# Performance work log

Measured on AMD Instinct MI355X. Metric: run time of the kernel, lower is better.

Reference implementation:

```python
import jax, jax.numpy as jnp
import numpy as np

# Fixed varlen layout: 2 sequences of length 2048 packed into N=4096 tokens
B, S, H, HK, D = 2, 2048, 32, 8, 128
G = H // HK  # GQA group size
SCALE = 1.0 / float(np.sqrt(D))


def setup_inputs() -> dict:
    key = jax.random.key(0)
    k0, k1, k2 = jax.random.split(key, 3)
    N = B * S
    return {
        "q": jax.random.normal(k0, (N, H, D), jnp.float32),
        "k": jax.random.normal(k1, (N, HK, D), jnp.float32),
        "v": jax.random.normal(k2, (N, HK, D), jnp.float32),
        "k_cache": jnp.zeros((N, HK * D), jnp.float32),
        "v_cache": jnp.zeros((N, HK * D), jnp.float32),
        "slot_mapping": jnp.arange(N, dtype=jnp.int32),
    }


def reference(q, k, v, k_cache, v_cache, slot_mapping):
    N = q.shape[0]
    num_slots = k_cache.shape[0]
    # --- store_kvcache: scatter flattened K/V rows into paged slots; slot==-1 skipped ---
    safe = jnp.where(slot_mapping >= 0, slot_mapping, num_slots)  # out-of-range -> dropped
    k_cache_new = k_cache.at[safe].set(k.reshape(N, HK * D), mode="drop")
    v_cache_new = v_cache.at[safe].set(v.reshape(N, HK * D), mode="drop")
    # --- prefill path (block_tables=None): causal varlen attention on fresh k,v ---
    qb = q.reshape(B, S, HK, G, D)
    kb = k.reshape(B, S, HK, D)
    vb = v.reshape(B, S, HK, D)
    scores = jnp.einsum("bqhgd,bkhd->bhgqk", qb, kb) * SCALE  # [B,HK,G,S,S]
    causal = jnp.tril(jnp.ones((S, S), dtype=bool))
    scores = jnp.where(causal, scores, jnp.finfo(scores.dtype).min)
    p = jax.nn.softmax(scores, axis=-1)
    o = jnp.einsum("bhgqk,bkhd->bqhgd", p, vb).reshape(N, H, D)
    return o, k_cache_new, v_cache_new
```

## Files before the change

### kernel.cpp

```cpp
#include <hip/hip_runtime.h>
#include <stdint.h>
#include <math.h>

constexpr int B = 2, S = 2048, H = 32, HK = 8, D = 128;
constexpr int N = B * S;
constexpr int KVD = HK * D;
constexpr float SCALE = 0.08838834764831845f;
constexpr float LOG2E = 1.4426950408889634f;
constexpr float QSCALE = SCALE * LOG2E;
constexpr float CSHIFT = 8.0f;

typedef __attribute__((ext_vector_type(8))) short short8;
typedef __attribute__((ext_vector_type(4))) float floatx4;

static __device__ __forceinline__ uint32_t f2bf1(float f) {
    union { float f; uint32_t u; } c; c.f = f;
    return (c.u + 0x7FFFu + ((c.u >> 16) & 1u)) >> 16;
}
static __device__ __forceinline__ uint32_t packbf(float a, float b) {
    return f2bf1(a) | (f2bf1(b) << 16);
}
static __device__ __forceinline__ uint32_t fbits(float f) {
    union { float f; uint32_t u; } c; c.f = f; return c.u;
}
static __device__ __forceinline__ uint32_t packtrunc(float lo, float hi) {
    return __builtin_amdgcn_perm(fbits(hi), fbits(lo), 0x07060302u);
}
static __device__ __forceinline__ void load_lds16(const void* g, void* l) {
    __builtin_amdgcn_global_load_lds((const __attribute__((address_space(1))) uint32_t*)g,
                                     (__attribute__((address_space(3))) uint32_t*)l,
                                     16, 0, 0);
}

__global__ __launch_bounds__(256) void k_prep(const float* __restrict__ k,
                                              const int* __restrict__ slot_mapping,
                                              float* __restrict__ kc_out,
                                              uint16_t* __restrict__ Kb) {
    int tid = blockIdx.x * 256 + threadIdx.x;
    int idx = tid * 4;
    int token = idx >> 10;
    int rem = idx & 1023;
    float4 val = *(const float4*)(k + idx);
    int s = slot_mapping[token];
    if (s >= 0 && s < N) {
        *(float4*)(kc_out + (size_t)s * KVD + rem) = val;
    }
    int b  = token >> 11;
    int ss = token & 2047;
    int hk = rem >> 7;
    int d  = rem & 127;
    uint2 pk;
    pk.x = packbf(val.x, val.y);
    pk.y = packbf(val.z, val.w);
    *(uint2*)(Kb + (((size_t)(b * HK + hk) * S + ss) * D + d)) = pk;
}

__global__ __launch_bounds__(256) void v_prep(const float* __restrict__ v,
                                              const int* __restrict__ slot_mapping,
                                              float* __restrict__ vc_out,
                                              uint16_t* __restrict__ Vt) {
    __shared__ float tile[64][129];
    int t = threadIdx.x;
    int kv0 = blockIdx.x * 64;
    int bhk = blockIdx.y;
    int b = bhk >> 3, hk = bhk & 7;

#pragma unroll
    for (int i = 0; i < 8; ++i) {
        int r = i * 8 + (t >> 5);
        int c = (t & 31) * 4;
        int token = b * S + kv0 + r;
        float4 val = *(const float4*)(v + (size_t)token * KVD + hk * D + c);
        int s = slot_mapping[token];
        if (s >= 0 && s < N) {
            *(float4*)(vc_out + (size_t)s * KVD + hk * D + c) = val;
        }
        tile[r][c + 0] = val.x; tile[r][c + 1] = val.y;
        tile[r][c + 2] = val.z; tile[r][c + 3] = val.w;
    }
    __syncthreads();
#pragma unroll
    for (int i = 0; i < 8; ++i) {
        int d = i * 16 + (t >> 4);
        int c = (t & 15) * 4;
        uint2 pk;
        pk.x = packbf(tile[c + 0][d], tile[c + 1][d]);
        pk.y = packbf(tile[c + 2][d], tile[c + 3][d]);
        *(uint2*)(Vt + ((size_t)(bhk * D + d)) * S + kv0 + c) = pk;
    }
}

__global__ __launch_bounds__(512, 2) void attn(const float* __restrict__ q,
                                               const uint16_t* __restrict__ Kb,
                                               const uint16_t* __restrict__ Vt,
                                               float* __restrict__ out) {
    __shared__ uint16_t sK[2][64 * 128];
    __shared__ uint16_t sV[2][128 * 64];

    int id = blockIdx.x;
    int hk = id & 7;
    int s0 = id >> 3;
    int x  = s0 & 7;
    int g2 = (s0 >> 3) & 1;
    int b  = s0 >> 4;
    int h0 = hk * 4 + g2 * 2;

    int t = threadIdx.x;
    int lane = t & 63, wave = t >> 6;
    int quad = lane >> 4, n = lane & 15, xr = n & 7;

    const uint16_t* Kbh = Kb + (size_t)(b * HK + hk) * S * D;
    const uint16_t* Vbh = Vt + (size_t)(b * HK + hk) * D * S;

    const uint16_t* gK[2]; const uint16_t* gV[2];
    int oK[2], oV[2];
#pragma unroll
    for (int j = 0; j < 2; ++j) {
        int i = wave * 2 + j;
        int rK = i * 4 + (lane >> 4);
        int cK = ((lane & 15) ^ (rK & 7)) * 8;
        gK[j] = Kbh + (size_t)rK * D + cK;
        oK[j] = i * 512;
        int rV = i * 8 + (lane >> 3);
        int cV = ((lane & 7) ^ (rV & 7)) * 8;
        gV[j] = Vbh + (size_t)rV * S + cV;
        oV[j] = i * 512;
    }

    for (int pass = 0; pass < 2; ++pass) {
        int qt = pass ? x : 15 - x;
        int q0 = qt * 128;
        int qwave = q0 + wave * 16;

        short8 bq[2][4];
#pragma unroll
        for (int g = 0; g < 2; ++g) {
            const float* qrow = q + (size_t)(b * S + qwave + n) * (H * D) + (h0 + g) * D + quad * 8;
#pragma unroll
            for (int kc = 0; kc < 4; ++kc) {
                float4 v0 = *(const float4*)(qrow + kc * 32);
                float4 v1 = *(const float4*)(qrow + kc * 32 + 4);
                uint4 pk;
                pk.x = packtrunc(v0.x * QSCALE, v0.y * QSCALE);
                pk.y = packtrunc(v0.z * QSCALE, v0.w * QSCALE);
                pk.z = packtrunc(v1.x * QSCALE, v1.y * QSCALE);
                pk.w = packtrunc(v1.z * QSCALE, v1.w * QSCALE);
                bq[g][kc] = *(short8*)&pk;
            }
        }

        floatx4 o_acc[2][8];
#pragma unroll
        for (int g = 0; g < 2; ++g)
#pragma unroll
            for (int i = 0; i < 8; ++i) o_acc[g][i] = (floatx4){0.f, 0.f, 0.f, 0.f};
        float lsum[2] = {0.f, 0.f};

        int nt = 2 * qt + 2;
        __syncthreads();
#pragma unroll
        for (int j = 0; j < 2; ++j) load_lds16(gK[j], &sK[0][0] + oK[j]);
#pragma unroll
        for (int j = 0; j < 2; ++j) load_lds16(gV[j], &sV[0][0] + oV[j]);

        for (int tile = 0; tile < nt; ++tile) {
            int cur = tile & 1;
            __syncthreads();
            if (tile + 1 < nt) {
                int kvn = (tile + 1) * 64;
#pragma unroll
                for (int j = 0; j < 2; ++j) load_lds16(gK[j] + (size_t)kvn * D, &sK[cur ^ 1][0] + oK[j]);
#pragma unroll
                for (int j = 0; j < 2; ++j) load_lds16(gV[j] + kvn, &sV[cur ^ 1][0] + oV[j]);
            }
            int kv0 = tile * 64;
            if (kv0 > qwave + 15) continue;

            const uint16_t* K_ = &sK[cur][0];
            const uint16_t* V_ = &sV[cur][0];

            floatx4 acc[2][4];
#pragma unroll
            for (int g = 0; g < 2; ++g)
#pragma unroll
                for (int sub = 0; sub < 4; ++sub) acc[g][sub] = (floatx4){0.f, 0.f, 0.f, 0.f};
#pragma unroll
            for (int sub = 0; sub < 4; ++sub) {
#pragma unroll
                for (int kc = 0; kc < 4; ++kc) {
                    short8 ak = *(const short8*)(K_ + (sub * 16 + n) * 128 + (((kc * 4 + quad) ^ xr) * 8));
                    acc[0][sub] = __builtin_amdgcn_mfma_f32_16x16x32_bf16(ak, bq[0][kc], acc[0][sub], 0, 0, 0);
                    acc[1][sub] = __builtin_amdgcn_mfma_f32_16x16x32_bf16(ak, bq[1][kc], acc[1][sub], 0, 0, 0);
                }
            }

            short8 ap[2][2];
            int qg = qwave + n;
            if (kv0 + 63 > qwave) {
#pragma unroll
                for (int sub = 0; sub < 4; ++sub)
#pragma unroll
                    for (int reg = 0; reg < 4; ++reg)
                        if (kv0 + sub * 16 + quad * 4 + reg > qg) {
                            acc[0][sub][reg] = -1e9f;
                            acc[1][sub][reg] = -1e9f;
                        }
            }
#pragma unroll
            for (int g = 0; g < 2; ++g) {
                float rs = 0.f;
                uint32_t pw[4][2];
#pragma unroll
                for (int sub = 0; sub < 4; ++sub) {
                    float p0 = exp2f(acc[g][sub][0] - CSHIFT);
                    float p1 = exp2f(acc[g][sub][1] - CSHIFT);
                    float p2 = exp2f(acc[g][sub][2] - CSHIFT);
                    float p3 = exp2f(acc[g][sub][3] - CSHIFT);
                    rs += (p0 + p1) + (p2 + p3);
                    pw[sub][0] = packtrunc(p0, p1);
                    pw[sub][1] = packtrunc(p2, p3);
                }
                lsum[g] += rs;

#pragma unroll
                for (int ks = 0; ks < 2; ++ks) {
                    uint32_t x0 = pw[2 * ks][0],     x1 = pw[2 * ks][1];
                    uint32_t y0 = pw[2 * ks + 1][0], y1 = pw[2 * ks + 1][1];
                    asm("v_permlane32_swap_b32 %0, %1" : "+v"(x0), "+v"(y0));
                    asm("v_permlane32_swap_b32 %0, %1" : "+v"(x1), "+v"(y1));
                    asm("v_permlane16_swap_b32 %0, %1" : "+v"(x0), "+v"(y0));
                    asm("v_permlane16_swap_b32 %0, %1" : "+v"(x1), "+v"(y1));
                    uint4 w; w.x = x0; w.y = x1; w.z = y0; w.w = y1;
                    ap[g][ks] = *(short8*)&w;
                }
            }

#pragma unroll
            for (int d8 = 0; d8 < 8; ++d8) {
#pragma unroll
                for (int ks = 0; ks < 2; ++ks) {
                    short8 bv = *(const short8*)(V_ + (d8 * 16 + n) * 64 + (((ks * 4 + quad) ^ xr) * 8));
                    o_acc[0][d8] = __builtin_amdgcn_mfma_f32_16x16x32_bf16(ap[0][ks], bv, o_acc[0][d8], 0, 0, 0);
                    o_acc[1][d8] = __builtin_amdgcn_mfma_f32_16x16x32_bf16(ap[1][ks], bv, o_acc[1][d8], 0, 0, 0);
                }
            }
        }

#pragma unroll
        for (int g = 0; g < 2; ++g) {
            float s = lsum[g];
            s += __shfl_xor(s, 16);
            s += __shfl_xor(s, 32);
            float linv = 1.0f / s;
            float lr[4];
#pragma unroll
            for (int reg = 0; reg < 4; ++reg) lr[reg] = __shfl(linv, quad * 4 + reg);
#pragma unroll
            for (int d8 = 0; d8 < 8; ++d8) {
#pragma unroll
                for (int reg = 0; reg < 4; ++reg) {
                    size_t row = (size_t)(b * S + qwave + quad * 4 + reg);
                    out[row * (H * D) + (h0 + g) * D + d8 * 16 + n] = o_acc[g][d8][reg] * lr[reg];
                }
            }
        }
    }
}

extern "C" void kernel_launch(void* const* d_in, const int* in_sizes, int n_in,
                              void* d_out, int out_size, void* d_ws, size_t ws_size,
                              hipStream_t stream) {
    const float* q = (const float*)d_in[0];
    const float* k = (const float*)d_in[1];
    const float* v = (const float*)d_in[2];
    const int* slot_mapping = (const int*)d_in[5];

    float* o_out  = (float*)d_out;
    float* kc_out = o_out + (size_t)N * H * D;
    float* vc_out = kc_out + (size_t)N * KVD;

    uint16_t* Kb = (uint16_t*)d_ws;
    uint16_t* Vt = Kb + (size_t)B * HK * S * D;

    k_prep<<<(N * KVD / 4) / 256, 256, 0, stream>>>(k, slot_mapping, kc_out, Kb);
    v_prep<<<dim3(S / 64, B * HK), 256, 0, stream>>>(v, slot_mapping, vc_out, Vt);
    attn<<<dim3(256), 512, 0, stream>>>(q, Kb, Vt, o_out);
}
```

Before: 282.3 us.

## Software-pipeline QK and softmax-PV across 32-wide KV tiles with 4-buffer LDS

Shrinks KV tiles from 64 to 32 rows, keeps four LDS buffers, and interleaves the QK^T MFMA of one tile with the softmax and PV of the previous tile, so exp and VALU work can overlap matrix-core work. The V tile layout and swizzle are changed to fit the narrower tile, and each wave now issues a single global-to-LDS load per tile. This adds twice as many barriers per KV row and more register pressure from the two live score accumulators, which could hurt occupancy at 2 blocks of 512 threads.

```diff
diff --git a/kernel.cpp b/kernel.cpp
--- a/kernel.cpp
+++ b/kernel.cpp
@@ -94,8 +94,8 @@
                                                const uint16_t* __restrict__ Kb,
                                                const uint16_t* __restrict__ Vt,
                                                float* __restrict__ out) {
-    __shared__ uint16_t sK[2][64 * 128];
-    __shared__ uint16_t sV[2][128 * 64];
+    __shared__ uint16_t sK[4][32 * 128];
+    __shared__ uint16_t sV[4][128 * 32];
 
     int id = blockIdx.x;
     int hk = id & 7;
@@ -112,20 +112,14 @@
     const uint16_t* Kbh = Kb + (size_t)(b * HK + hk) * S * D;
     const uint16_t* Vbh = Vt + (size_t)(b * HK + hk) * D * S;
 
-    const uint16_t* gK[2]; const uint16_t* gV[2];
-    int oK[2], oV[2];
-#pragma unroll
-    for (int j = 0; j < 2; ++j) {
-        int i = wave * 2 + j;
-        int rK = i * 4 + (lane >> 4);
-        int cK = ((lane & 15) ^ (rK & 7)) * 8;
-        gK[j] = Kbh + (size_t)rK * D + cK;
-        oK[j] = i * 512;
-        int rV = i * 8 + (lane >> 3);
-        int cV = ((lane & 7) ^ (rV & 7)) * 8;
-        gV[j] = Vbh + (size_t)rV * S + cV;
-        oV[j] = i * 512;
-    }
+    int rK = wave * 4 + (lane >> 4);
+    int cK = ((lane & 15) ^ (rK & 7)) * 8;
+    const uint16_t* gK = Kbh + (size_t)rK * D + cK;
+    int oK = wave * 512;
+    int rV = wave * 16 + (lane >> 2);
+    int cV = ((lane & 3) ^ ((lane >> 3) & 3)) * 8;
+    const uint16_t* gV = Vbh + (size_t)rV * S + cV;
+    int oV = wave * 512;
 
     for (int pass = 0; pass < 2; ++pass) {
         int qt = pass ? x : 15 - x;
@@ -156,36 +150,22 @@
             for (int i = 0; i < 8; ++i) o_acc[g][i] = (floatx4){0.f, 0.f, 0.f, 0.f};
         float lsum[2] = {0.f, 0.f};
 
-        int nt = 2 * qt + 2;
-        __syncthreads();
-#pragma unroll
-        for (int j = 0; j < 2; ++j) load_lds16(gK[j], &sK[0][0] + oK[j]);
-#pragma unroll
-        for (int j = 0; j < 2; ++j) load_lds16(gV[j], &sV[0][0] + oV[j]);
-
-        for (int tile = 0; tile < nt; ++tile) {
-            int cur = tile & 1;
-            __syncthreads();
-            if (tile + 1 < nt) {
-                int kvn = (tile + 1) * 64;
-#pragma unroll
-                for (int j = 0; j < 2; ++j) load_lds16(gK[j] + (size_t)kvn * D, &sK[cur ^ 1][0] + oK[j]);
-#pragma unroll
-                for (int j = 0; j < 2; ++j) load_lds16(gV[j] + kvn, &sV[cur ^ 1][0] + oV[j]);
-            }
-            int kv0 = tile * 64;
-            if (kv0 > qwave + 15) continue;
-
-            const uint16_t* K_ = &sK[cur][0];
-            const uint16_t* V_ = &sV[cur][0];
-
-            floatx4 acc[2][4];
+        auto STAGE = [&](int tile) {
+            int buf = tile & 3;
+            size_t kvn = (size_t)tile * 32;
+            load_lds16(gK + kvn * D, &sK[buf][0] + oK);
+            load_lds16(gV + kvn, &sV[buf][0] + oV);
+        };
+        auto QK = [&](int tile, floatx4 (&acc)[2][2]) {
+            int kv0 = tile * 32;
 #pragma unroll
             for (int g = 0; g < 2; ++g)
 #pragma unroll
-                for (int sub = 0; sub < 4; ++sub) acc[g][sub] = (floatx4){0.f, 0.f, 0.f, 0.f};
-#pragma unroll
-            for (int sub = 0; sub < 4; ++sub) {
+                for (int sub = 0; sub < 2; ++sub) acc[g][sub] = (floatx4){0.f, 0.f, 0.f, 0.f};
+            if (kv0 > qwave + 15) return;
+            const uint16_t* K_ = &sK[tile & 3][0];
+#pragma unroll
+            for (int sub = 0; sub < 2; ++sub) {
 #pragma unroll
                 for (int kc = 0; kc < 4; ++kc) {
                     short8 ak = *(const short8*)(K_ + (sub * 16 + n) * 128 + (((kc * 4 + quad) ^ xr) * 8));
@@ -193,12 +173,15 @@
                     acc[1][sub] = __builtin_amdgcn_mfma_f32_16x16x32_bf16(ak, bq[1][kc], acc[1][sub], 0, 0, 0);
                 }
             }
-
-            short8 ap[2][2];
+        };
+        auto SMPV = [&](int tile, floatx4 (&acc)[2][2]) {
+            int kv0 = tile * 32;
+            if (kv0 > qwave + 15) return;
+            const uint16_t* V_ = &sV[tile & 3][0];
             int qg = qwave + n;
-            if (kv0 + 63 > qwave) {
-#pragma unroll
-                for (int sub = 0; sub < 4; ++sub)
+            if (kv0 + 31 > qwave) {
+#pragma unroll
+                for (int sub = 0; sub < 2; ++sub)
 #pragma unroll
                     for (int reg = 0; reg < 4; ++reg)
                         if (kv0 + sub * 16 + quad * 4 + reg > qg) {
@@ -206,12 +189,13 @@
                             acc[1][sub][reg] = -1e9f;
                         }
             }
+            short8 ap[2];
 #pragma unroll
             for (int g = 0; g < 2; ++g) {
                 float rs = 0.f;
-                uint32_t pw[4][2];
-#pragma unroll
-                for (int sub = 0; sub < 4; ++sub) {
+                uint32_t pw[2][2];
+#pragma unroll
+                for (int sub = 0; sub < 2; ++sub) {
                     float p0 = exp2f(acc[g][sub][0] - CSHIFT);
                     float p1 = exp2f(acc[g][sub][1] - CSHIFT);
                     float p2 = exp2f(acc[g][sub][2] - CSHIFT);
@@ -221,30 +205,41 @@
                     pw[sub][1] = packtrunc(p2, p3);
                 }
                 lsum[g] += rs;
-
-#pragma unroll
-                for (int ks = 0; ks < 2; ++ks) {
-                    uint32_t x0 = pw[2 * ks][0],     x1 = pw[2 * ks][1];
-                    uint32_t y0 = pw[2 * ks + 1][0], y1 = pw[2 * ks + 1][1];
-                    asm("v_permlane32_swap_b32 %0, %1" : "+v"(x0), "+v"(y0));
-                    asm("v_permlane32_swap_b32 %0, %1" : "+v"(x1), "+v"(y1));
-                    asm("v_permlane16_swap_b32 %0, %1" : "+v"(x0), "+v"(y0));
-                    asm("v_permlane16_swap_b32 %0, %1" : "+v"(x1), "+v"(y1));
-                    uint4 w; w.x = x0; w.y = x1; w.z = y0; w.w = y1;
-                    ap[g][ks] = *(short8*)&w;
-                }
-            }
-
+                uint32_t x0 = pw[0][0], x1 = pw[0][1];
+                uint32_t y0 = pw[1][0], y1 = pw[1][1];
+                asm("v_permlane32_swap_b32 %0, %1" : "+v"(x0), "+v"(y0));
+                asm("v_permlane32_swap_b32 %0, %1" : "+v"(x1), "+v"(y1));
+                asm("v_permlane16_swap_b32 %0, %1" : "+v"(x0), "+v"(y0));
+                asm("v_permlane16_swap_b32 %0, %1" : "+v"(x1), "+v"(y1));
+                uint4 w; w.x = x0; w.y = x1; w.z = y0; w.w = y1;
+                ap[g] = *(short8*)&w;
+            }
 #pragma unroll
             for (int d8 = 0; d8 < 8; ++d8) {
-#pragma unroll
-                for (int ks = 0; ks < 2; ++ks) {
-                    short8 bv = *(const short8*)(V_ + (d8 * 16 + n) * 64 + (((ks * 4 + quad) ^ xr) * 8));
-                    o_acc[0][d8] = __builtin_amdgcn_mfma_f32_16x16x32_bf16(ap[0][ks], bv, o_acc[0][d8], 0, 0, 0);
-                    o_acc[1][d8] = __builtin_amdgcn_mfma_f32_16x16x32_bf16(ap[1][ks], bv, o_acc[1][d8], 0, 0, 0);
-                }
-            }
-        }
+                short8 bv = *(const short8*)(V_ + (d8 * 16 + n) * 32 + ((quad ^ ((n >> 1) & 3)) * 8));
+                o_acc[0][d8] = __builtin_amdgcn_mfma_f32_16x16x32_bf16(ap[0], bv, o_acc[0][d8], 0, 0, 0);
+                o_acc[1][d8] = __builtin_amdgcn_mfma_f32_16x16x32_bf16(ap[1], bv, o_acc[1][d8], 0, 0, 0);
+            }
+        };
+
+        int nt = 4 * qt + 4;
+        __syncthreads();
+        STAGE(0);
+
+        floatx4 accA[2][2], accB[2][2];
+
+        for (int tt = 0; tt < nt; tt += 2) {
+            __syncthreads();
+            if (tt + 1 < nt) STAGE(tt + 1);
+            QK(tt, accA);
+            if (tt > 0) SMPV(tt - 1, accB);
+
+            __syncthreads();
+            if (tt + 2 < nt) STAGE(tt + 2);
+            QK(tt + 1, accB);
+            SMPV(tt, accA);
+        }
+        SMPV(nt - 1, accB);
 
 #pragma unroll
         for (int g = 0; g < 2; ++g) {
```

Result: slower. 292.4 us (+3.6%).
